# Kernel tuning notes

Measured on AMD Instinct MI355X. Metric: run time of the kernel, lower is better.

The kernel has to match this reference:

```python
import jax, jax.numpy as jnp
import numpy as np

DIM = 512
NUM_HEADS = 8
HEAD_DIM = DIM // NUM_HEADS
SCALE = HEAD_DIM ** -0.5
B, N, K_HOPS = 16, 1024, 5


def setup_inputs() -> dict:
    key = jax.random.key(0)
    ks = jax.random.split(key, 7)
    x = jax.random.normal(ks[0], (B, N, DIM), jnp.float32)
    Hstack = jax.random.uniform(ks[1], (K_HOPS, N, N), jnp.float32)
    hop_logits_attn = jax.random.normal(ks[2], (NUM_HEADS, K_HOPS), jnp.float32)
    rel_alpha = jax.random.normal(ks[3], (NUM_HEADS,), jnp.float32)
    Wqkv = jax.random.normal(ks[4], (3 * DIM, DIM), jnp.float32) * 0.02
    Wproj = jax.random.normal(ks[5], (DIM, DIM), jnp.float32) * 0.02
    bproj = jax.random.normal(ks[6], (DIM,), jnp.float32) * 0.02
    return {"x": x, "Hstack": Hstack, "hop_logits_attn": hop_logits_attn,
            "rel_alpha": rel_alpha, "Wqkv": Wqkv, "Wproj": Wproj, "bproj": bproj}


def reference(x, Hstack, hop_logits_attn, rel_alpha, Wqkv, Wproj, bproj):
    bs, n_tok, c_dim = x.shape
    # qkv projection: [B,N,3C] -> [3,B,H,N,hd]
    qkv = (x @ Wqkv.T).reshape(bs, n_tok, 3, NUM_HEADS, c_dim // NUM_HEADS)
    qkv = qkv.transpose(2, 0, 3, 1, 4)
    q, k, v = qkv[0], qkv[1], qkv[2]
    logits = jnp.einsum('bhnd,bhmd->bhnm', q, k) * SCALE  # [B,H,N,N]
    # hop-distance bias: per-head softmax mixture over K hop matrices
    w = jax.nn.softmax(hop_logits_attn, axis=-1)          # [H,K]
    B_head = jnp.einsum('hk,kij->hij', w, Hstack)          # [H,N,N]
    attn_bias = rel_alpha[:, None, None] * B_head          # [H,N,N]
    attn = jax.nn.softmax(logits + attn_bias[None], axis=-1)
    out = jnp.einsum('bhnm,bhmd->bhnd', attn, v)           # [B,H,N,hd]
    out = out.transpose(0, 2, 1, 3).reshape(bs, n_tok, c_dim)
    return out @ Wproj.T + bproj
```

## Files before the change

### kernel.cpp

```cpp
#include <hip/hip_runtime.h>
#include <hip/hip_bf16.h>
#include <hip/hip_fp16.h>
#include <stdint.h>

#define DIM   512
#define NH    8
#define HD    64
#define NB    16
#define NTOK  1024
#define KHOPS 5

typedef __attribute__((ext_vector_type(8))) short bf16x8;
typedef __attribute__((ext_vector_type(4))) float f32x4;

#define LOG2E 1.4426950408889634f

__device__ __forceinline__ unsigned short f32_to_bf16(float f) {
    unsigned int u = __builtin_bit_cast(unsigned int, f);
    unsigned int r = (u + 0x7FFFu + ((u >> 16) & 1u)) >> 16;
    return (unsigned short)r;
}

__device__ __forceinline__ float fast_exp2(float x) {
    return __builtin_amdgcn_exp2f(x);
}

#define AS1C(p) ((const __attribute__((address_space(1))) void*)(p))
#define AS3(p)  ((__attribute__((address_space(3))) void*)(p))

__global__ __launch_bounds__(256) void cvt_f32_bf16(const float* __restrict__ in,
                                                    unsigned short* __restrict__ out, int n4) {
    int i = blockIdx.x * 256 + threadIdx.x;
    if (i < n4) {
        float4 v = reinterpret_cast<const float4*>(in)[i];
        ushort4 o;
        o.x = f32_to_bf16(v.x); o.y = f32_to_bf16(v.y);
        o.z = f32_to_bf16(v.z); o.w = f32_to_bf16(v.w);
        reinterpret_cast<ushort4*>(out)[i] = o;
    }
}

__global__ __launch_bounds__(256) void transpose_f32(const float* __restrict__ in,
                                                     float* __restrict__ outp) {
    __shared__ float Ts[64][65];
    const int tid = threadIdx.x;
    const int jt = blockIdx.x, it = blockIdx.y, k = blockIdx.z;
    const float* src = in + (size_t)k * 1048576 + (size_t)(it * 64) * 1024 + jt * 64;
    float* dst = outp + (size_t)k * 1048576 + (size_t)(jt * 64) * 1024 + it * 64;
    const int r = tid >> 2, c4 = tid & 3;
#pragma unroll
    for (int t = 0; t < 4; ++t) {
        int c = (c4 + t * 4) * 4;
        float4 v = *reinterpret_cast<const float4*>(src + (size_t)r * 1024 + c);
        Ts[r][c] = v.x; Ts[r][c + 1] = v.y; Ts[r][c + 2] = v.z; Ts[r][c + 3] = v.w;
    }
    __syncthreads();
#pragma unroll
    for (int t = 0; t < 4; ++t) {
        int c = (c4 + t * 4) * 4;
        float4 v;
        v.x = Ts[c][r]; v.y = Ts[c + 1][r]; v.z = Ts[c + 2][r]; v.w = Ts[c + 3][r];
        *reinterpret_cast<float4*>(dst + (size_t)r * 1024 + c) = v;
    }
}

__global__ __launch_bounds__(256) void bias_combine(const float* __restrict__ Ht,
                                                    const float* __restrict__ hop_logits,
                                                    const float* __restrict__ rel_alpha,
                                                    uint32_t* __restrict__ biast) {
    __shared__ float coef[NH][KHOPS];
    int tid = threadIdx.x;
    if (tid < NH) {
        float m = -1e30f;
        for (int k = 0; k < KHOPS; ++k) m = fmaxf(m, hop_logits[tid * KHOPS + k]);
        float e[KHOPS]; float s = 0.f;
        for (int k = 0; k < KHOPS; ++k) {
            e[k] = fast_exp2((hop_logits[tid * KHOPS + k] - m) * LOG2E);
            s += e[k];
        }
        float ra = rel_alpha[tid] * LOG2E / s;
        for (int k = 0; k < KHOPS; ++k) coef[tid][k] = ra * e[k];
    }
    __syncthreads();
    int o2 = blockIdx.x * 256 + tid;
    int iw2  = o2 & 15;
    int j    = (o2 >> 4) & 1023;
    int it32 = (o2 >> 14) & 31;
    int h    = o2 >> 19;
    const float2* H2 = reinterpret_cast<const float2*>(Ht);
    size_t src = (size_t)j * 512 + it32 * 16 + iw2;
    float2 h0 = H2[src];
    float2 h1 = H2[524288 + src];
    float2 h2 = H2[2 * 524288 + src];
    float2 h3 = H2[3 * 524288 + src];
    float2 h4 = H2[4 * 524288 + src];
    float vx = coef[h][0] * h0.x + coef[h][1] * h1.x + coef[h][2] * h2.x +
               coef[h][3] * h3.x + coef[h][4] * h4.x;
    float vy = coef[h][0] * h0.y + coef[h][1] * h1.y + coef[h][2] * h2.y +
               coef[h][3] * h3.y + coef[h][4] * h4.y;
    __half2 hv = __floats2half2_rn(vx, vy);
    biast[o2] = __builtin_bit_cast(uint32_t, hv);
}

template <bool BF16_OUT>
__global__ __launch_bounds__(256) void gemm_bt(const unsigned short* __restrict__ A,
                                               const unsigned short* __restrict__ Bw,
                                               void* __restrict__ Cout,
                                               const float* __restrict__ cbias,
                                               int M, int Nn, int K) {
    __shared__ unsigned short As[128 * 32];
    __shared__ unsigned short Bs[128 * 32];
    const int tid  = threadIdx.x;
    const int lane = tid & 63;
    const int w    = tid >> 6;
    const int wr   = (w >> 1) * 64, wc = (w & 1) * 64;
    const int l15  = lane & 15, quad = lane >> 4;
    const int m0   = blockIdx.x * 128, n0 = blockIdx.y * 128;

    f32x4 acc[4][4];
#pragma unroll
    for (int i = 0; i < 4; ++i)
#pragma unroll
        for (int j = 0; j < 4; ++j) { acc[i][j][0] = 0.f; acc[i][j][1] = 0.f; acc[i][j][2] = 0.f; acc[i][j][3] = 0.f; }

    for (int k0 = 0; k0 < K; k0 += 32) {
        __syncthreads();
#pragma unroll
        for (int t = 0; t < 2; ++t) {
            int c = t * 256 + w * 64 + lane;
            int r = c >> 2, kh = c & 3;
            const unsigned short* ga = A  + (size_t)(m0 + r) * K + k0 + kh * 8;
            const unsigned short* gb = Bw + (size_t)(n0 + r) * K + k0 + kh * 8;
            __builtin_amdgcn_global_load_lds(AS1C(ga), AS3(&As[(t * 256 + w * 64) * 8]), 16, 0, 0);
            __builtin_amdgcn_global_load_lds(AS1C(gb), AS3(&Bs[(t * 256 + w * 64) * 8]), 16, 0, 0);
        }
        __syncthreads();
        bf16x8 af[4], bfr[4];
#pragma unroll
        for (int rt = 0; rt < 4; ++rt)
            af[rt] = *reinterpret_cast<const bf16x8*>(&As[(wr + rt * 16 + l15) * 32 + quad * 8]);
#pragma unroll
        for (int ct = 0; ct < 4; ++ct)
            bfr[ct] = *reinterpret_cast<const bf16x8*>(&Bs[(wc + ct * 16 + l15) * 32 + quad * 8]);
#pragma unroll
        for (int rt = 0; rt < 4; ++rt)
#pragma unroll
            for (int ct = 0; ct < 4; ++ct)
                acc[rt][ct] = __builtin_amdgcn_mfma_f32_16x16x32_bf16(af[rt], bfr[ct], acc[rt][ct], 0, 0, 0);
    }

    if (BF16_OUT) {
        unsigned short* C = (unsigned short*)Cout;
#pragma unroll
        for (int rt = 0; rt < 4; ++rt)
#pragma unroll
            for (int ct = 0; ct < 4; ++ct)
#pragma unroll
                for (int reg = 0; reg < 4; ++reg) {
                    int row = m0 + wr + rt * 16 + quad * 4 + reg;
                    int col = n0 + wc + ct * 16 + l15;
                    C[(size_t)row * Nn + col] = f32_to_bf16(acc[rt][ct][reg]);
                }
    } else {
        float* C = (float*)Cout;
#pragma unroll
        for (int ct = 0; ct < 4; ++ct) {
            int col = n0 + wc + ct * 16 + l15;
            float bv = cbias[col];
#pragma unroll
            for (int rt = 0; rt < 4; ++rt)
#pragma unroll
                for (int reg = 0; reg < 4; ++reg) {
                    int row = m0 + wr + rt * 16 + quad * 4 + reg;
                    C[(size_t)row * Nn + col] = acc[rt][ct][reg] + bv;
                }
        }
    }
}

__global__ __launch_bounds__(256) void transpose_v(const unsigned short* __restrict__ qkv,
                                                   unsigned short* __restrict__ vt) {
    __shared__ unsigned short Ts[64 * 66];
    const int tid = threadIdx.x;
    const int jt = blockIdx.x, h = blockIdx.y, b = blockIdx.z;
    const int j0 = jt * 64;
#pragma unroll
    for (int t = 0; t < 2; ++t) {
        int c = t * 256 + tid;
        int j = c >> 3, dh = c & 7;
        const uint32_t* g = reinterpret_cast<const uint32_t*>(
            qkv + (size_t)(b * 1024 + j0 + j) * 1536 + 1024 + h * 64 + dh * 8);
        uint32_t d0 = g[0], d1 = g[1], d2 = g[2], d3 = g[3];
        uint32_t* ls = reinterpret_cast<uint32_t*>(&Ts[j * 66 + dh * 8]);
        ls[0] = d0; ls[1] = d1; ls[2] = d2; ls[3] = d3;
    }
    __syncthreads();
#pragma unroll
    for (int t = 0; t < 2; ++t) {
        int c = t * 256 + tid;
        int d = c >> 3, jh = c & 7;
        unsigned short tmp[8];
#pragma unroll
        for (int e = 0; e < 8; ++e) tmp[e] = Ts[(jh * 8 + e) * 66 + d];
        uint32_t o0 = (uint32_t)tmp[0] | ((uint32_t)tmp[1] << 16);
        uint32_t o1 = (uint32_t)tmp[2] | ((uint32_t)tmp[3] << 16);
        uint32_t o2 = (uint32_t)tmp[4] | ((uint32_t)tmp[5] << 16);
        uint32_t o3 = (uint32_t)tmp[6] | ((uint32_t)tmp[7] << 16);
        uint32_t* gout = reinterpret_cast<uint32_t*>(
            vt + ((size_t)((b * 8 + h) * 64 + d)) * 1024 + j0 + jh * 8);
        gout[0] = o0; gout[1] = o1; gout[2] = o2; gout[3] = o3;
    }
}

__global__ __launch_bounds__(256, 3) void flash_attn(const unsigned short* __restrict__ qkv,
                                                     const unsigned short* __restrict__ vt,
                                                     const unsigned short* __restrict__ biast,
                                                     unsigned short* __restrict__ aout) {
    __shared__ unsigned short Kb[64 * 64];
    __shared__ unsigned short Vb[64 * 64];
    __shared__ unsigned short Ps[4 * 32 * 72];
    const int tid  = threadIdx.x;
    const int lane = tid & 63, w = tid >> 6;
    const int l15  = lane & 15, quad = lane >> 4;
    const int qt = blockIdx.x, h = blockIdx.y, b = blockIdx.z;
    const int i0 = qt * 128 + w * 32;
    const float kscale = 0.125f * LOG2E;
    const int l7 = l15 & 7;

    bf16x8 qf[2][2];
#pragma unroll
    for (int rt = 0; rt < 2; ++rt)
#pragma unroll
        for (int ks = 0; ks < 2; ++ks)
            qf[rt][ks] = *reinterpret_cast<const bf16x8*>(
                qkv + (size_t)(b * 1024 + i0 + rt * 16 + l15) * 1536 + h * 64 + ks * 32 + quad * 8);

    f32x4 o[2][4];
    f32x4 lacc[2];
#pragma unroll
    for (int rt = 0; rt < 2; ++rt) {
#pragma unroll
        for (int nt = 0; nt < 4; ++nt) { o[rt][nt][0] = 0.f; o[rt][nt][1] = 0.f; o[rt][nt][2] = 0.f; o[rt][nt][3] = 0.f; }
        lacc[rt][0] = 0.f; lacc[rt][1] = 0.f; lacc[rt][2] = 0.f; lacc[rt][3] = 0.f;
    }

    bf16x8 ones;
#pragma unroll
    for (int e = 0; e < 8; ++e) ones[e] = (short)0x3F80;

    const int srow = lane >> 3;
    const int gch  = (lane & 7) ^ (srow & 7);
    const unsigned short* kgbase = qkv + (size_t)b * 1024 * 1536 + 512 + h * 64 + gch * 8;
    const unsigned short* vgbase = vt + (size_t)((b * 8 + h) * 64) * 1024 + gch * 8;
    const unsigned short* bb = biast + ((size_t)(h * 32 + qt * 4 + w) * 1024) * 32 + quad * 4;
    unsigned short* ps = &Ps[w * 32 * 72];

    for (int j0 = 0; j0 < 1024; j0 += 64) {
        __syncthreads();
#pragma unroll
        for (int t = 0; t < 2; ++t) {
            int rl = w * 16 + t * 8 + srow;
            __builtin_amdgcn_global_load_lds(AS1C(kgbase + (size_t)(j0 + rl) * 1536),
                                             AS3(&Kb[(w * 16 + t * 8) * 64]), 16, 0, 0);
            __builtin_amdgcn_global_load_lds(AS1C(vgbase + (size_t)rl * 1024 + j0),
                                             AS3(&Vb[(w * 16 + t * 8) * 64]), 16, 0, 0);
        }
        uint2 bl[2][4];
#pragma unroll
        for (int rt = 0; rt < 2; ++rt)
#pragma unroll
            for (int jt = 0; jt < 4; ++jt)
                bl[rt][jt] = *reinterpret_cast<const uint2*>(
                    bb + (size_t)(j0 + jt * 16 + l15) * 32 + rt * 16);
        __syncthreads();

        f32x4 s[2][4];
#pragma unroll
        for (int rt = 0; rt < 2; ++rt)
#pragma unroll
            for (int jt = 0; jt < 4; ++jt) { s[rt][jt][0] = 0.f; s[rt][jt][1] = 0.f; s[rt][jt][2] = 0.f; s[rt][jt][3] = 0.f; }
#pragma unroll
        for (int ks = 0; ks < 2; ++ks) {
            bf16x8 kf[4];
#pragma unroll
            for (int jt = 0; jt < 4; ++jt)
                kf[jt] = *reinterpret_cast<const bf16x8*>(
                    &Kb[(jt * 16 + l15) * 64 + (((ks * 4 + quad) ^ l7) * 8)]);
#pragma unroll
            for (int rt = 0; rt < 2; ++rt)
#pragma unroll
                for (int jt = 0; jt < 4; ++jt)
                    s[rt][jt] = __builtin_amdgcn_mfma_f32_16x16x32_bf16(qf[rt][ks], kf[jt], s[rt][jt], 0, 0, 0);
        }

#pragma unroll
        for (int rt = 0; rt < 2; ++rt)
#pragma unroll
            for (int jt = 0; jt < 4; ++jt) {
                float2 f0 = __half22float2(__builtin_bit_cast(__half2, bl[rt][jt].x));
                float2 f1 = __half22float2(__builtin_bit_cast(__half2, bl[rt][jt].y));
                float bvr[4] = {f0.x, f0.y, f1.x, f1.y};
#pragma unroll
                for (int reg = 0; reg < 4; ++reg) {
                    float p = fast_exp2(__builtin_fmaf(s[rt][jt][reg], kscale, bvr[reg]));
                    ps[(rt * 16 + quad * 4 + reg) * 72 + jt * 16 + l15] = f32_to_bf16(p);
                }
            }

#pragma unroll
        for (int ks = 0; ks < 2; ++ks) {
            bf16x8 pf[2], vf[4];
#pragma unroll
            for (int rt = 0; rt < 2; ++rt)
                pf[rt] = *reinterpret_cast<const bf16x8*>(ps + (rt * 16 + l15) * 72 + ks * 32 + quad * 8);
#pragma unroll
            for (int nt = 0; nt < 4; ++nt)
                vf[nt] = *reinterpret_cast<const bf16x8*>(
                    &Vb[(nt * 16 + l15) * 64 + (((ks * 4 + quad) ^ l7) * 8)]);
#pragma unroll
            for (int rt = 0; rt < 2; ++rt) {
#pragma unroll
                for (int nt = 0; nt < 4; ++nt)
                    o[rt][nt] = __builtin_amdgcn_mfma_f32_16x16x32_bf16(pf[rt], vf[nt], o[rt][nt], 0, 0, 0);
                lacc[rt] = __builtin_amdgcn_mfma_f32_16x16x32_bf16(pf[rt], ones, lacc[rt], 0, 0, 0);
            }
        }
    }

#pragma unroll
    for (int rt = 0; rt < 2; ++rt) {
        float inv[4];
#pragma unroll
        for (int reg = 0; reg < 4; ++reg) inv[reg] = 1.f / lacc[rt][reg];
#pragma unroll
        for (int nt = 0; nt < 4; ++nt)
#pragma unroll
            for (int reg = 0; reg < 4; ++reg) {
                int row = b * 1024 + i0 + rt * 16 + quad * 4 + reg;
                int col = h * 64 + nt * 16 + l15;
                aout[(size_t)row * 512 + col] = f32_to_bf16(o[rt][nt][reg] * inv[reg]);
            }
    }
}

extern "C" void kernel_launch(void* const* d_in, const int* in_sizes, int n_in,
                              void* d_out, int out_size, void* d_ws, size_t ws_size,
                              hipStream_t stream) {
    const float* x          = (const float*)d_in[0];
    const float* Hstack     = (const float*)d_in[1];
    const float* hop_logits = (const float*)d_in[2];
    const float* rel_alpha  = (const float*)d_in[3];
    const float* Wqkv       = (const float*)d_in[4];
    const float* Wproj      = (const float*)d_in[5];
    const float* bproj      = (const float*)d_in[6];
    float* out = (float*)d_out;

    char* ws = (char*)d_ws;
    unsigned short* xb    = (unsigned short*)(ws);
    unsigned short* wqb   = (unsigned short*)(ws + 16777216);
    unsigned short* wpb   = (unsigned short*)(ws + 18350080);
    unsigned short* qkvb  = (unsigned short*)(ws + 18874368);
    unsigned short* vtb   = (unsigned short*)(ws + 69206016);
    unsigned short* biast = (unsigned short*)(ws + 85983232);
    float*          Ht    = (float*)(ws + 102760448);
    unsigned short* aoutb = (unsigned short*)(ws + 102760448);

    cvt_f32_bf16<<<8192, 256, 0, stream>>>(x, xb, 2097152);
    cvt_f32_bf16<<<768, 256, 0, stream>>>(Wqkv, wqb, 196608);
    cvt_f32_bf16<<<256, 256, 0, stream>>>(Wproj, wpb, 65536);

    transpose_f32<<<dim3(16, 16, 5), 256, 0, stream>>>(Hstack, Ht);
    bias_combine<<<16384, 256, 0, stream>>>(Ht, hop_logits, rel_alpha, (uint32_t*)biast);

    gemm_bt<true><<<dim3(128, 12), 256, 0, stream>>>(xb, wqb, qkvb, nullptr, 16384, 1536, 512);

    transpose_v<<<dim3(16, 8, 16), 256, 0, stream>>>(qkvb, vtb);

    flash_attn<<<dim3(8, 8, 16), 256, 0, stream>>>(qkvb, vtb, biast, aoutb);

    gemm_bt<false><<<dim3(128, 4), 256, 0, stream>>>(aoutb, wpb, out, bproj, 16384, 512, 512);
}
```

Before: 267.7 us.

## Fuse hop-bias transpose/combine and double-buffer K/V in larger flash-attention tiles

Merges the Hstack transpose and the per-head bias combine into a single kernel. It reads Hstack directly in its original layout and transposes the half-precision result through LDS, which avoids writing and re-reading a full fp32 transposed copy. The flash attention kernel now processes 64 query rows per wave (256 per block), halving the grid and doubling K/V reuse. It also double-buffers the K/V LDS tiles and the bias registers so the next tile's loads overlap the current tile's compute. The cost is higher register and LDS use, so occupancy drops from 3 to 2 blocks per CU, and with half as many blocks the GPU may be less full.

```diff
diff --git a/kernel.cpp b/kernel.cpp
--- a/kernel.cpp
+++ b/kernel.cpp
@@ -40,66 +40,59 @@
     }
 }
 
-__global__ __launch_bounds__(256) void transpose_f32(const float* __restrict__ in,
-                                                     float* __restrict__ outp) {
-    __shared__ float Ts[64][65];
+__global__ __launch_bounds__(256) void bias_fused(const float* __restrict__ H,
+                                                  const float* __restrict__ hop_logits,
+                                                  const float* __restrict__ rel_alpha,
+                                                  uint32_t* __restrict__ biast) {
+    __shared__ unsigned short Ls[64 * 76];
     const int tid = threadIdx.x;
-    const int jt = blockIdx.x, it = blockIdx.y, k = blockIdx.z;
-    const float* src = in + (size_t)k * 1048576 + (size_t)(it * 64) * 1024 + jt * 64;
-    float* dst = outp + (size_t)k * 1048576 + (size_t)(jt * 64) * 1024 + it * 64;
-    const int r = tid >> 2, c4 = tid & 3;
-#pragma unroll
-    for (int t = 0; t < 4; ++t) {
-        int c = (c4 + t * 4) * 4;
-        float4 v = *reinterpret_cast<const float4*>(src + (size_t)r * 1024 + c);
-        Ts[r][c] = v.x; Ts[r][c + 1] = v.y; Ts[r][c + 2] = v.z; Ts[r][c + 3] = v.w;
+    const int jt = blockIdx.x, it = blockIdx.y, h = blockIdx.z;
+    const int j0 = jt * 64, i0 = it * 64;
+    float cf[KHOPS];
+    {
+        float m = -1e30f;
+#pragma unroll
+        for (int k = 0; k < KHOPS; ++k) m = fmaxf(m, hop_logits[h * KHOPS + k]);
+        float s = 0.f;
+#pragma unroll
+        for (int k = 0; k < KHOPS; ++k) { cf[k] = fast_exp2((hop_logits[h * KHOPS + k] - m) * LOG2E); s += cf[k]; }
+        float ra = rel_alpha[h] * LOG2E / s;
+#pragma unroll
+        for (int k = 0; k < KHOPS; ++k) cf[k] *= ra;
+    }
+    const int r = tid >> 2, c0 = (tid & 3) * 16;
+    float acc[16];
+#pragma unroll
+    for (int e = 0; e < 16; ++e) acc[e] = 0.f;
+    for (int k = 0; k < KHOPS; ++k) {
+        const float4* src = reinterpret_cast<const float4*>(
+            H + (size_t)k * 1048576 + (size_t)(i0 + r) * 1024 + j0 + c0);
+#pragma unroll
+        for (int q = 0; q < 4; ++q) {
+            float4 v = src[q];
+            acc[q * 4 + 0] += cf[k] * v.x; acc[q * 4 + 1] += cf[k] * v.y;
+            acc[q * 4 + 2] += cf[k] * v.z; acc[q * 4 + 3] += cf[k] * v.w;
+        }
+    }
+#pragma unroll
+    for (int q = 0; q < 4; ++q) {
+        __half2 p0 = __floats2half2_rn(acc[q * 4 + 0], acc[q * 4 + 1]);
+        __half2 p1 = __floats2half2_rn(acc[q * 4 + 2], acc[q * 4 + 3]);
+        uint32_t* d = reinterpret_cast<uint32_t*>(&Ls[r * 76 + c0 + q * 4]);
+        d[0] = __builtin_bit_cast(uint32_t, p0);
+        d[1] = __builtin_bit_cast(uint32_t, p1);
     }
     __syncthreads();
-#pragma unroll
-    for (int t = 0; t < 4; ++t) {
-        int c = (c4 + t * 4) * 4;
-        float4 v;
-        v.x = Ts[c][r]; v.y = Ts[c + 1][r]; v.z = Ts[c + 2][r]; v.w = Ts[c + 3][r];
-        *reinterpret_cast<float4*>(dst + (size_t)r * 1024 + c) = v;
-    }
-}
-
-__global__ __launch_bounds__(256) void bias_combine(const float* __restrict__ Ht,
-                                                    const float* __restrict__ hop_logits,
-                                                    const float* __restrict__ rel_alpha,
-                                                    uint32_t* __restrict__ biast) {
-    __shared__ float coef[NH][KHOPS];
-    int tid = threadIdx.x;
-    if (tid < NH) {
-        float m = -1e30f;
-        for (int k = 0; k < KHOPS; ++k) m = fmaxf(m, hop_logits[tid * KHOPS + k]);
-        float e[KHOPS]; float s = 0.f;
-        for (int k = 0; k < KHOPS; ++k) {
-            e[k] = fast_exp2((hop_logits[tid * KHOPS + k] - m) * LOG2E);
-            s += e[k];
-        }
-        float ra = rel_alpha[tid] * LOG2E / s;
-        for (int k = 0; k < KHOPS; ++k) coef[tid][k] = ra * e[k];
-    }
-    __syncthreads();
-    int o2 = blockIdx.x * 256 + tid;
-    int iw2  = o2 & 15;
-    int j    = (o2 >> 4) & 1023;
-    int it32 = (o2 >> 14) & 31;
-    int h    = o2 >> 19;
-    const float2* H2 = reinterpret_cast<const float2*>(Ht);
-    size_t src = (size_t)j * 512 + it32 * 16 + iw2;
-    float2 h0 = H2[src];
-    float2 h1 = H2[524288 + src];
-    float2 h2 = H2[2 * 524288 + src];
-    float2 h3 = H2[3 * 524288 + src];
-    float2 h4 = H2[4 * 524288 + src];
-    float vx = coef[h][0] * h0.x + coef[h][1] * h1.x + coef[h][2] * h2.x +
-               coef[h][3] * h3.x + coef[h][4] * h4.x;
-    float vy = coef[h][0] * h0.y + coef[h][1] * h1.y + coef[h][2] * h2.y +
-               coef[h][3] * h3.y + coef[h][4] * h4.y;
-    __half2 hv = __floats2half2_rn(vx, vy);
-    biast[o2] = __builtin_bit_cast(uint32_t, hv);
+    const int iw2 = tid & 15, jl = tid >> 4;
+#pragma unroll
+    for (int g = 0; g < 2; ++g)
+#pragma unroll
+        for (int t = 0; t < 4; ++t) {
+            int j = t * 16 + jl;
+            int i = g * 32 + iw2 * 2;
+            uint32_t lo = (uint32_t)Ls[i * 76 + j] | ((uint32_t)Ls[(i + 1) * 76 + j] << 16);
+            biast[(size_t)((h * 32 + (i0 >> 5) + g) * 1024 + (j0 + j)) * 16 + iw2] = lo;
+        }
 }
 
 template <bool BF16_OUT>
@@ -212,33 +205,32 @@
     }
 }
 
-__global__ __launch_bounds__(256, 3) void flash_attn(const unsigned short* __restrict__ qkv,
+__global__ __launch_bounds__(256, 2) void flash_attn(const unsigned short* __restrict__ qkv,
                                                      const unsigned short* __restrict__ vt,
                                                      const unsigned short* __restrict__ biast,
                                                      unsigned short* __restrict__ aout) {
-    __shared__ unsigned short Kb[64 * 64];
-    __shared__ unsigned short Vb[64 * 64];
-    __shared__ unsigned short Ps[4 * 32 * 72];
+    __shared__ unsigned short Kb[2][64 * 64];
+    __shared__ unsigned short Vb[2][64 * 64];
+    __shared__ unsigned short Ps[4][64 * 72];
     const int tid  = threadIdx.x;
     const int lane = tid & 63, w = tid >> 6;
-    const int l15  = lane & 15, quad = lane >> 4;
+    const int l15  = lane & 15, quad = lane >> 4, l7 = l15 & 7;
     const int qt = blockIdx.x, h = blockIdx.y, b = blockIdx.z;
-    const int i0 = qt * 128 + w * 32;
+    const int i0 = qt * 256 + w * 64;
     const float kscale = 0.125f * LOG2E;
-    const int l7 = l15 & 7;
-
-    bf16x8 qf[2][2];
-#pragma unroll
-    for (int rt = 0; rt < 2; ++rt)
+
+    bf16x8 qf[4][2];
+#pragma unroll
+    for (int rt = 0; rt < 4; ++rt)
 #pragma unroll
         for (int ks = 0; ks < 2; ++ks)
             qf[rt][ks] = *reinterpret_cast<const bf16x8*>(
                 qkv + (size_t)(b * 1024 + i0 + rt * 16 + l15) * 1536 + h * 64 + ks * 32 + quad * 8);
 
-    f32x4 o[2][4];
-    f32x4 lacc[2];
-#pragma unroll
-    for (int rt = 0; rt < 2; ++rt) {
+    f32x4 o[4][4];
+    f32x4 lacc[4];
+#pragma unroll
+    for (int rt = 0; rt < 4; ++rt) {
 #pragma unroll
         for (int nt = 0; nt < 4; ++nt) { o[rt][nt][0] = 0.f; o[rt][nt][1] = 0.f; o[rt][nt][2] = 0.f; o[rt][nt][3] = 0.f; }
         lacc[rt][0] = 0.f; lacc[rt][1] = 0.f; lacc[rt][2] = 0.f; lacc[rt][3] = 0.f;
@@ -249,86 +241,109 @@
     for (int e = 0; e < 8; ++e) ones[e] = (short)0x3F80;
 
     const int srow = lane >> 3;
-    const int gch  = (lane & 7) ^ (srow & 7);
+    const int gch  = (lane & 7) ^ srow;
     const unsigned short* kgbase = qkv + (size_t)b * 1024 * 1536 + 512 + h * 64 + gch * 8;
     const unsigned short* vgbase = vt + (size_t)((b * 8 + h) * 64) * 1024 + gch * 8;
-    const unsigned short* bb = biast + ((size_t)(h * 32 + qt * 4 + w) * 1024) * 32 + quad * 4;
-    unsigned short* ps = &Ps[w * 32 * 72];
-
-    for (int j0 = 0; j0 < 1024; j0 += 64) {
+    const unsigned short* bb = biast + (size_t)(h * 32 + qt * 8 + w * 2) * 32768 + quad * 4;
+    unsigned short* ps = &Ps[w][0];
+
+    uint2 bl[2][4][4];
+#pragma unroll
+    for (int t = 0; t < 2; ++t) {
+        int rl = w * 16 + t * 8 + srow;
+        __builtin_amdgcn_global_load_lds(AS1C(kgbase + (size_t)rl * 1536),
+                                         AS3(&Kb[0][(w * 16 + t * 8) * 64]), 16, 0, 0);
+        __builtin_amdgcn_global_load_lds(AS1C(vgbase + (size_t)rl * 1024),
+                                         AS3(&Vb[0][(w * 16 + t * 8) * 64]), 16, 0, 0);
+    }
+#pragma unroll
+    for (int rt = 0; rt < 4; ++rt)
+#pragma unroll
+        for (int jt = 0; jt < 4; ++jt)
+            bl[0][rt][jt] = *reinterpret_cast<const uint2*>(
+                bb + (rt >> 1) * 32768 + (size_t)(jt * 16 + l15) * 32 + (rt & 1) * 16);
+
+#pragma unroll 2
+    for (int it = 0; it < 16; ++it) {
+        const int cur = it & 1, nxt = cur ^ 1;
+        const int j0 = it * 64;
         __syncthreads();
-#pragma unroll
-        for (int t = 0; t < 2; ++t) {
-            int rl = w * 16 + t * 8 + srow;
-            __builtin_amdgcn_global_load_lds(AS1C(kgbase + (size_t)(j0 + rl) * 1536),
-                                             AS3(&Kb[(w * 16 + t * 8) * 64]), 16, 0, 0);
-            __builtin_amdgcn_global_load_lds(AS1C(vgbase + (size_t)rl * 1024 + j0),
-                                             AS3(&Vb[(w * 16 + t * 8) * 64]), 16, 0, 0);
-        }
-        uint2 bl[2][4];
-#pragma unroll
-        for (int rt = 0; rt < 2; ++rt)
-#pragma unroll
-            for (int jt = 0; jt < 4; ++jt)
-                bl[rt][jt] = *reinterpret_cast<const uint2*>(
-                    bb + (size_t)(j0 + jt * 16 + l15) * 32 + rt * 16);
-        __syncthreads();
-
-        f32x4 s[2][4];
-#pragma unroll
-        for (int rt = 0; rt < 2; ++rt)
-#pragma unroll
-            for (int jt = 0; jt < 4; ++jt) { s[rt][jt][0] = 0.f; s[rt][jt][1] = 0.f; s[rt][jt][2] = 0.f; s[rt][jt][3] = 0.f; }
+
+        if (it < 15) {
+            const int j0n = j0 + 64;
+#pragma unroll
+            for (int t = 0; t < 2; ++t) {
+                int rl = w * 16 + t * 8 + srow;
+                __builtin_amdgcn_global_load_lds(AS1C(kgbase + (size_t)(j0n + rl) * 1536),
+                                                 AS3(&Kb[nxt][(w * 16 + t * 8) * 64]), 16, 0, 0);
+                __builtin_amdgcn_global_load_lds(AS1C(vgbase + (size_t)rl * 1024 + j0n),
+                                                 AS3(&Vb[nxt][(w * 16 + t * 8) * 64]), 16, 0, 0);
+            }
+#pragma unroll
+            for (int rt = 0; rt < 4; ++rt)
+#pragma unroll
+                for (int jt = 0; jt < 4; ++jt)
+                    bl[nxt][rt][jt] = *reinterpret_cast<const uint2*>(
+                        bb + (rt >> 1) * 32768 + (size_t)(j0n + jt * 16 + l15) * 32 + (rt & 1) * 16);
+        }
+
+#pragma unroll
+        for (int rth = 0; rth < 2; ++rth) {
+            f32x4 s[2][4];
+#pragma unroll
+            for (int r2 = 0; r2 < 2; ++r2)
+#pragma unroll
+                for (int jt = 0; jt < 4; ++jt) { s[r2][jt][0] = 0.f; s[r2][jt][1] = 0.f; s[r2][jt][2] = 0.f; s[r2][jt][3] = 0.f; }
+#pragma unroll
+            for (int ks = 0; ks < 2; ++ks) {
+                bf16x8 kf[4];
+#pragma unroll
+                for (int jt = 0; jt < 4; ++jt)
+                    kf[jt] = *reinterpret_cast<const bf16x8*>(
+                        &Kb[cur][(jt * 16 + l15) * 64 + (((ks * 4 + quad) ^ l7) * 8)]);
+#pragma unroll
+                for (int r2 = 0; r2 < 2; ++r2)
+#pragma unroll
+                    for (int jt = 0; jt < 4; ++jt)
+                        s[r2][jt] = __builtin_amdgcn_mfma_f32_16x16x32_bf16(qf[rth * 2 + r2][ks], kf[jt], s[r2][jt], 0, 0, 0);
+            }
+#pragma unroll
+            for (int r2 = 0; r2 < 2; ++r2) {
+                const int rt = rth * 2 + r2;
+#pragma unroll
+                for (int jt = 0; jt < 4; ++jt) {
+                    float2 f0 = __half22float2(__builtin_bit_cast(__half2, bl[cur][rt][jt].x));
+                    float2 f1 = __half22float2(__builtin_bit_cast(__half2, bl[cur][rt][jt].y));
+                    float bvr[4] = {f0.x, f0.y, f1.x, f1.y};
+#pragma unroll
+                    for (int reg = 0; reg < 4; ++reg) {
+                        float p = fast_exp2(__builtin_fmaf(s[r2][jt][reg], kscale, bvr[reg]));
+                        ps[(rt * 16 + quad * 4 + reg) * 72 + jt * 16 + l15] = f32_to_bf16(p);
+                    }
+                }
+            }
+        }
+
 #pragma unroll
         for (int ks = 0; ks < 2; ++ks) {
-            bf16x8 kf[4];
-#pragma unroll
-            for (int jt = 0; jt < 4; ++jt)
-                kf[jt] = *reinterpret_cast<const bf16x8*>(
-                    &Kb[(jt * 16 + l15) * 64 + (((ks * 4 + quad) ^ l7) * 8)]);
-#pragma unroll
-            for (int rt = 0; rt < 2; ++rt)
-#pragma unroll
-                for (int jt = 0; jt < 4; ++jt)
-                    s[rt][jt] = __builtin_amdgcn_mfma_f32_16x16x32_bf16(qf[rt][ks], kf[jt], s[rt][jt], 0, 0, 0);
-        }
-
-#pragma unroll
-        for (int rt = 0; rt < 2; ++rt)
-#pragma unroll
-            for (int jt = 0; jt < 4; ++jt) {
-                float2 f0 = __half22float2(__builtin_bit_cast(__half2, bl[rt][jt].x));
-                float2 f1 = __half22float2(__builtin_bit_cast(__half2, bl[rt][jt].y));
-                float bvr[4] = {f0.x, f0.y, f1.x, f1.y};
-#pragma unroll
-                for (int reg = 0; reg < 4; ++reg) {
-                    float p = fast_exp2(__builtin_fmaf(s[rt][jt][reg], kscale, bvr[reg]));
-                    ps[(rt * 16 + quad * 4 + reg) * 72 + jt * 16 + l15] = f32_to_bf16(p);
-                }
-            }
-
-#pragma unroll
-        for (int ks = 0; ks < 2; ++ks) {
-            bf16x8 pf[2], vf[4];
-#pragma unroll
-            for (int rt = 0; rt < 2; ++rt)
-                pf[rt] = *reinterpret_cast<const bf16x8*>(ps + (rt * 16 + l15) * 72 + ks * 32 + quad * 8);
+            bf16x8 vf[4];
 #pragma unroll
             for (int nt = 0; nt < 4; ++nt)
                 vf[nt] = *reinterpret_cast<const bf16x8*>(
-                    &Vb[(nt * 16 + l15) * 64 + (((ks * 4 + quad) ^ l7) * 8)]);
-#pragma unroll
-            for (int rt = 0; rt < 2; ++rt) {
+                    &Vb[cur][(nt * 16 + l15) * 64 + (((ks * 4 + quad) ^ l7) * 8)]);
+#pragma unroll
+            for (int rt = 0; rt < 4; ++rt) {
+                bf16x8 pf = *reinterpret_cast<const bf16x8*>(ps + (rt * 16 + l15) * 72 + ks * 32 + quad * 8);
 #pragma unroll
                 for (int nt = 0; nt < 4; ++nt)
-                    o[rt][nt] = __builtin_amdgcn_mfma_f32_16x16x32_bf16(pf[rt], vf[nt], o[rt][nt], 0, 0, 0);
-                lacc[rt] = __builtin_amdgcn_mfma_f32_16x16x32_bf16(pf[rt], ones, lacc[rt], 0, 0, 0);
-            }
-        }
-    }
-
-#pragma unroll
-    for (int rt = 0; rt < 2; ++rt) {
+                    o[rt][nt] = __builtin_amdgcn_mfma_f32_16x16x32_bf16(pf, vf[nt], o[rt][nt], 0, 0, 0);
+                lacc[rt] = __builtin_amdgcn_mfma_f32_16x16x32_bf16(pf, ones, lacc[rt], 0, 0, 0);
+            }
+        }
+    }
+
+#pragma unroll
+    for (int rt = 0; rt < 4; ++rt) {
         float inv[4];
 #pragma unroll
         for (int reg = 0; reg < 4; ++reg) inv[reg] = 1.f / lacc[rt][reg];
@@ -362,21 +377,19 @@
     unsigned short* qkvb  = (unsigned short*)(ws + 18874368);
     unsigned short* vtb   = (unsigned short*)(ws + 69206016);
     unsigned short* biast = (unsigned short*)(ws + 85983232);
-    float*          Ht    = (float*)(ws + 102760448);
     unsigned short* aoutb = (unsigned short*)(ws + 102760448);
 
     cvt_f32_bf16<<<8192, 256, 0, stream>>>(x, xb, 2097152);
     cvt_f32_bf16<<<768, 256, 0, stream>>>(Wqkv, wqb, 196608);
     cvt_f32_bf16<<<256, 256, 0, stream>>>(Wproj, wpb, 65536);
 
-    transpose_f32<<<dim3(16, 16, 5), 256, 0, stream>>>(Hstack, Ht);
-    bias_combine<<<16384, 256, 0, stream>>>(Ht, hop_logits, rel_alpha, (uint32_t*)biast);
+    bias_fused<<<dim3(16, 16, 8), 256, 0, stream>>>(Hstack, hop_logits, rel_alpha, (uint32_t*)biast);
 
     gemm_bt<true><<<dim3(128, 12), 256, 0, stream>>>(xb, wqb, qkvb, nullptr, 16384, 1536, 512);
 
     transpose_v<<<dim3(16, 8, 16), 256, 0, stream>>>(qkvb, vtb);
 
-    flash_attn<<<dim3(8, 8, 16), 256, 0, stream>>>(qkvb, vtb, biast, aoutb);
+    flash_attn<<<dim3(4, 8, 16), 256, 0, stream>>>(qkvb, vtb, biast, aoutb);
 
     gemm_bt<false><<<dim3(128, 4), 256, 0, stream>>>(aoutb, wpb, out, bproj, 16384, 512, 512);
 }
```

Result: slower. 273.1 us (+2.0%).

## Fuse conversion kernels, bias transpose-combine, and V transpose into GEMM epilogue

Applied to the files above, without the earlier changes.

Merges the three fp32-to-bf16 conversion launches into one kernel and replaces the Hstack transpose plus bias combine with a single tiled kernel. That kernel reads Hstack directly, mixes the hops per head in registers and transposes through LDS. The QKV GEMM now writes the V columns directly in transposed layout, removing the separate transpose_v pass and its extra read and write of V. The flash attention grid is reordered so head is the fastest-varying block index, which may improve bias and cache locality. Fewer launches and intermediate buffers remain, at the cost of strided 8-byte stores in the V epilogue, and bias_fused now rereads Hstack once per head.

```diff
diff --git a/kernel.cpp b/kernel.cpp
--- a/kernel.cpp
+++ b/kernel.cpp
@@ -28,86 +28,83 @@
 #define AS1C(p) ((const __attribute__((address_space(1))) void*)(p))
 #define AS3(p)  ((__attribute__((address_space(3))) void*)(p))
 
-__global__ __launch_bounds__(256) void cvt_f32_bf16(const float* __restrict__ in,
-                                                    unsigned short* __restrict__ out, int n4) {
-    int i = blockIdx.x * 256 + threadIdx.x;
-    if (i < n4) {
-        float4 v = reinterpret_cast<const float4*>(in)[i];
-        ushort4 o;
-        o.x = f32_to_bf16(v.x); o.y = f32_to_bf16(v.y);
-        o.z = f32_to_bf16(v.z); o.w = f32_to_bf16(v.w);
-        reinterpret_cast<ushort4*>(out)[i] = o;
-    }
-}
-
-__global__ __launch_bounds__(256) void transpose_f32(const float* __restrict__ in,
-                                                     float* __restrict__ outp) {
-    __shared__ float Ts[64][65];
+__global__ __launch_bounds__(256) void cvt_all(const float* __restrict__ x,
+                                               const float* __restrict__ wq,
+                                               const float* __restrict__ wp,
+                                               unsigned short* __restrict__ xb,
+                                               unsigned short* __restrict__ wqb,
+                                               unsigned short* __restrict__ wpb) {
+    int bid = blockIdx.x;
+    const float* in; unsigned short* out; int i;
+    if (bid < 8192)      { in = x;  out = xb;  i = bid * 256 + threadIdx.x; }
+    else if (bid < 8960) { in = wq; out = wqb; i = (bid - 8192) * 256 + threadIdx.x; }
+    else                 { in = wp; out = wpb; i = (bid - 8960) * 256 + threadIdx.x; }
+    float4 v = reinterpret_cast<const float4*>(in)[i];
+    ushort4 o;
+    o.x = f32_to_bf16(v.x); o.y = f32_to_bf16(v.y);
+    o.z = f32_to_bf16(v.z); o.w = f32_to_bf16(v.w);
+    reinterpret_cast<ushort4*>(out)[i] = o;
+}
+
+__global__ __launch_bounds__(256) void bias_fused(const float* __restrict__ H,
+                                                  const float* __restrict__ hop_logits,
+                                                  const float* __restrict__ rel_alpha,
+                                                  uint32_t* __restrict__ biast) {
+    __shared__ unsigned short Ls[64 * 76];
     const int tid = threadIdx.x;
-    const int jt = blockIdx.x, it = blockIdx.y, k = blockIdx.z;
-    const float* src = in + (size_t)k * 1048576 + (size_t)(it * 64) * 1024 + jt * 64;
-    float* dst = outp + (size_t)k * 1048576 + (size_t)(jt * 64) * 1024 + it * 64;
-    const int r = tid >> 2, c4 = tid & 3;
-#pragma unroll
-    for (int t = 0; t < 4; ++t) {
-        int c = (c4 + t * 4) * 4;
-        float4 v = *reinterpret_cast<const float4*>(src + (size_t)r * 1024 + c);
-        Ts[r][c] = v.x; Ts[r][c + 1] = v.y; Ts[r][c + 2] = v.z; Ts[r][c + 3] = v.w;
+    const int jt = blockIdx.x, it = blockIdx.y, h = blockIdx.z;
+    const int j0 = jt * 64, i0 = it * 64;
+    float cf[KHOPS];
+    {
+        float m = -1e30f;
+#pragma unroll
+        for (int k = 0; k < KHOPS; ++k) m = fmaxf(m, hop_logits[h * KHOPS + k]);
+        float s = 0.f;
+#pragma unroll
+        for (int k = 0; k < KHOPS; ++k) { cf[k] = fast_exp2((hop_logits[h * KHOPS + k] - m) * LOG2E); s += cf[k]; }
+        float ra = rel_alpha[h] * LOG2E / s;
+#pragma unroll
+        for (int k = 0; k < KHOPS; ++k) cf[k] *= ra;
+    }
+    const int r = tid >> 2, c0 = (tid & 3) * 16;
+    float acc[16];
+#pragma unroll
+    for (int e = 0; e < 16; ++e) acc[e] = 0.f;
+    for (int k = 0; k < KHOPS; ++k) {
+        const float4* src = reinterpret_cast<const float4*>(
+            H + (size_t)k * 1048576 + (size_t)(i0 + r) * 1024 + j0 + c0);
+#pragma unroll
+        for (int q = 0; q < 4; ++q) {
+            float4 v = src[q];
+            acc[q * 4 + 0] += cf[k] * v.x; acc[q * 4 + 1] += cf[k] * v.y;
+            acc[q * 4 + 2] += cf[k] * v.z; acc[q * 4 + 3] += cf[k] * v.w;
+        }
+    }
+#pragma unroll
+    for (int q = 0; q < 4; ++q) {
+        __half2 p0 = __floats2half2_rn(acc[q * 4 + 0], acc[q * 4 + 1]);
+        __half2 p1 = __floats2half2_rn(acc[q * 4 + 2], acc[q * 4 + 3]);
+        uint32_t* d = reinterpret_cast<uint32_t*>(&Ls[r * 76 + c0 + q * 4]);
+        d[0] = __builtin_bit_cast(uint32_t, p0);
+        d[1] = __builtin_bit_cast(uint32_t, p1);
     }
     __syncthreads();
-#pragma unroll
-    for (int t = 0; t < 4; ++t) {
-        int c = (c4 + t * 4) * 4;
-        float4 v;
-        v.x = Ts[c][r]; v.y = Ts[c + 1][r]; v.z = Ts[c + 2][r]; v.w = Ts[c + 3][r];
-        *reinterpret_cast<float4*>(dst + (size_t)r * 1024 + c) = v;
-    }
-}
-
-__global__ __launch_bounds__(256) void bias_combine(const float* __restrict__ Ht,
-                                                    const float* __restrict__ hop_logits,
-                                                    const float* __restrict__ rel_alpha,
-                                                    uint32_t* __restrict__ biast) {
-    __shared__ float coef[NH][KHOPS];
-    int tid = threadIdx.x;
-    if (tid < NH) {
-        float m = -1e30f;
-        for (int k = 0; k < KHOPS; ++k) m = fmaxf(m, hop_logits[tid * KHOPS + k]);
-        float e[KHOPS]; float s = 0.f;
-        for (int k = 0; k < KHOPS; ++k) {
-            e[k] = fast_exp2((hop_logits[tid * KHOPS + k] - m) * LOG2E);
-            s += e[k];
-        }
-        float ra = rel_alpha[tid] * LOG2E / s;
-        for (int k = 0; k < KHOPS; ++k) coef[tid][k] = ra * e[k];
-    }
-    __syncthreads();
-    int o2 = blockIdx.x * 256 + tid;
-    int iw2  = o2 & 15;
-    int j    = (o2 >> 4) & 1023;
-    int it32 = (o2 >> 14) & 31;
-    int h    = o2 >> 19;
-    const float2* H2 = reinterpret_cast<const float2*>(Ht);
-    size_t src = (size_t)j * 512 + it32 * 16 + iw2;
-    float2 h0 = H2[src];
-    float2 h1 = H2[524288 + src];
-    float2 h2 = H2[2 * 524288 + src];
-    float2 h3 = H2[3 * 524288 + src];
-    float2 h4 = H2[4 * 524288 + src];
-    float vx = coef[h][0] * h0.x + coef[h][1] * h1.x + coef[h][2] * h2.x +
-               coef[h][3] * h3.x + coef[h][4] * h4.x;
-    float vy = coef[h][0] * h0.y + coef[h][1] * h1.y + coef[h][2] * h2.y +
-               coef[h][3] * h3.y + coef[h][4] * h4.y;
-    __half2 hv = __floats2half2_rn(vx, vy);
-    biast[o2] = __builtin_bit_cast(uint32_t, hv);
-}
-
-template <bool BF16_OUT>
-__global__ __launch_bounds__(256) void gemm_bt(const unsigned short* __restrict__ A,
-                                               const unsigned short* __restrict__ Bw,
-                                               void* __restrict__ Cout,
-                                               const float* __restrict__ cbias,
-                                               int M, int Nn, int K) {
+    const int iw2 = tid & 15, jl = tid >> 4;
+#pragma unroll
+    for (int g = 0; g < 2; ++g)
+#pragma unroll
+        for (int t = 0; t < 4; ++t) {
+            int j = t * 16 + jl;
+            int i = g * 32 + iw2 * 2;
+            uint32_t lo = (uint32_t)Ls[i * 76 + j] | ((uint32_t)Ls[(i + 1) * 76 + j] << 16);
+            biast[(size_t)((h * 32 + (i0 >> 5) + g) * 1024 + (j0 + j)) * 16 + iw2] = lo;
+        }
+}
+
+__global__ __launch_bounds__(256) void gemm_qkv(const unsigned short* __restrict__ A,
+                                                const unsigned short* __restrict__ Bw,
+                                                unsigned short* __restrict__ qkv,
+                                                unsigned short* __restrict__ vt) {
     __shared__ unsigned short As[128 * 32];
     __shared__ unsigned short Bs[128 * 32];
     const int tid  = threadIdx.x;
@@ -116,6 +113,7 @@
     const int wr   = (w >> 1) * 64, wc = (w & 1) * 64;
     const int l15  = lane & 15, quad = lane >> 4;
     const int m0   = blockIdx.x * 128, n0 = blockIdx.y * 128;
+    const int K = 512, Nn = 1536;
 
     f32x4 acc[4][4];
 #pragma unroll
@@ -149,8 +147,7 @@
                 acc[rt][ct] = __builtin_amdgcn_mfma_f32_16x16x32_bf16(af[rt], bfr[ct], acc[rt][ct], 0, 0, 0);
     }
 
-    if (BF16_OUT) {
-        unsigned short* C = (unsigned short*)Cout;
+    if (n0 < 1024) {
 #pragma unroll
         for (int rt = 0; rt < 4; ++rt)
 #pragma unroll
@@ -159,56 +156,85 @@
                 for (int reg = 0; reg < 4; ++reg) {
                     int row = m0 + wr + rt * 16 + quad * 4 + reg;
                     int col = n0 + wc + ct * 16 + l15;
-                    C[(size_t)row * Nn + col] = f32_to_bf16(acc[rt][ct][reg]);
+                    qkv[(size_t)row * Nn + col] = f32_to_bf16(acc[rt][ct][reg]);
                 }
     } else {
-        float* C = (float*)Cout;
+        const int b = m0 >> 10;
 #pragma unroll
         for (int ct = 0; ct < 4; ++ct) {
-            int col = n0 + wc + ct * 16 + l15;
-            float bv = cbias[col];
-#pragma unroll
-            for (int rt = 0; rt < 4; ++rt)
-#pragma unroll
-                for (int reg = 0; reg < 4; ++reg) {
-                    int row = m0 + wr + rt * 16 + quad * 4 + reg;
-                    C[(size_t)row * Nn + col] = acc[rt][ct][reg] + bv;
-                }
-        }
-    }
-}
-
-__global__ __launch_bounds__(256) void transpose_v(const unsigned short* __restrict__ qkv,
-                                                   unsigned short* __restrict__ vt) {
-    __shared__ unsigned short Ts[64 * 66];
-    const int tid = threadIdx.x;
-    const int jt = blockIdx.x, h = blockIdx.y, b = blockIdx.z;
-    const int j0 = jt * 64;
-#pragma unroll
-    for (int t = 0; t < 2; ++t) {
-        int c = t * 256 + tid;
-        int j = c >> 3, dh = c & 7;
-        const uint32_t* g = reinterpret_cast<const uint32_t*>(
-            qkv + (size_t)(b * 1024 + j0 + j) * 1536 + 1024 + h * 64 + dh * 8);
-        uint32_t d0 = g[0], d1 = g[1], d2 = g[2], d3 = g[3];
-        uint32_t* ls = reinterpret_cast<uint32_t*>(&Ts[j * 66 + dh * 8]);
-        ls[0] = d0; ls[1] = d1; ls[2] = d2; ls[3] = d3;
-    }
-    __syncthreads();
-#pragma unroll
-    for (int t = 0; t < 2; ++t) {
-        int c = t * 256 + tid;
-        int d = c >> 3, jh = c & 7;
-        unsigned short tmp[8];
-#pragma unroll
-        for (int e = 0; e < 8; ++e) tmp[e] = Ts[(jh * 8 + e) * 66 + d];
-        uint32_t o0 = (uint32_t)tmp[0] | ((uint32_t)tmp[1] << 16);
-        uint32_t o1 = (uint32_t)tmp[2] | ((uint32_t)tmp[3] << 16);
-        uint32_t o2 = (uint32_t)tmp[4] | ((uint32_t)tmp[5] << 16);
-        uint32_t o3 = (uint32_t)tmp[6] | ((uint32_t)tmp[7] << 16);
-        uint32_t* gout = reinterpret_cast<uint32_t*>(
-            vt + ((size_t)((b * 8 + h) * 64 + d)) * 1024 + j0 + jh * 8);
-        gout[0] = o0; gout[1] = o1; gout[2] = o2; gout[3] = o3;
+            int c = n0 - 1024 + wc + ct * 16 + l15;
+            unsigned short* vrow = vt + ((size_t)(b * 8) * 64 + c) * 1024;
+#pragma unroll
+            for (int rt = 0; rt < 4; ++rt) {
+                int trow = (m0 & 1023) + wr + rt * 16 + quad * 4;
+                ushort4 pk;
+                pk.x = f32_to_bf16(acc[rt][ct][0]);
+                pk.y = f32_to_bf16(acc[rt][ct][1]);
+                pk.z = f32_to_bf16(acc[rt][ct][2]);
+                pk.w = f32_to_bf16(acc[rt][ct][3]);
+                *reinterpret_cast<ushort4*>(vrow + trow) = pk;
+            }
+        }
+    }
+}
+
+__global__ __launch_bounds__(256) void gemm_proj(const unsigned short* __restrict__ A,
+                                                 const unsigned short* __restrict__ Bw,
+                                                 float* __restrict__ C,
+                                                 const float* __restrict__ cbias,
+                                                 int M, int Nn, int K) {
+    __shared__ unsigned short As[128 * 32];
+    __shared__ unsigned short Bs[128 * 32];
+    const int tid  = threadIdx.x;
+    const int lane = tid & 63;
+    const int w    = tid >> 6;
+    const int wr   = (w >> 1) * 64, wc = (w & 1) * 64;
+    const int l15  = lane & 15, quad = lane >> 4;
+    const int m0   = blockIdx.x * 128, n0 = blockIdx.y * 128;
+
+    f32x4 acc[4][4];
+#pragma unroll
+    for (int i = 0; i < 4; ++i)
+#pragma unroll
+        for (int j = 0; j < 4; ++j) { acc[i][j][0] = 0.f; acc[i][j][1] = 0.f; acc[i][j][2] = 0.f; acc[i][j][3] = 0.f; }
+
+    for (int k0 = 0; k0 < K; k0 += 32) {
+        __syncthreads();
+#pragma unroll
+        for (int t = 0; t < 2; ++t) {
+            int c = t * 256 + w * 64 + lane;
+            int r = c >> 2, kh = c & 3;
+            const unsigned short* ga = A  + (size_t)(m0 + r) * K + k0 + kh * 8;
+            const unsigned short* gb = Bw + (size_t)(n0 + r) * K + k0 + kh * 8;
+            __builtin_amdgcn_global_load_lds(AS1C(ga), AS3(&As[(t * 256 + w * 64) * 8]), 16, 0, 0);
+            __builtin_amdgcn_global_load_lds(AS1C(gb), AS3(&Bs[(t * 256 + w * 64) * 8]), 16, 0, 0);
+        }
+        __syncthreads();
+        bf16x8 af[4], bfr[4];
+#pragma unroll
+        for (int rt = 0; rt < 4; ++rt)
+            af[rt] = *reinterpret_cast<const bf16x8*>(&As[(wr + rt * 16 + l15) * 32 + quad * 8]);
+#pragma unroll
+        for (int ct = 0; ct < 4; ++ct)
+            bfr[ct] = *reinterpret_cast<const bf16x8*>(&Bs[(wc + ct * 16 + l15) * 32 + quad * 8]);
+#pragma unroll
+        for (int rt = 0; rt < 4; ++rt)
+#pragma unroll
+            for (int ct = 0; ct < 4; ++ct)
+                acc[rt][ct] = __builtin_amdgcn_mfma_f32_16x16x32_bf16(af[rt], bfr[ct], acc[rt][ct], 0, 0, 0);
+    }
+
+#pragma unroll
+    for (int ct = 0; ct < 4; ++ct) {
+        int col = n0 + wc + ct * 16 + l15;
+        float bv = cbias[col];
+#pragma unroll
+        for (int rt = 0; rt < 4; ++rt)
+#pragma unroll
+            for (int reg = 0; reg < 4; ++reg) {
+                int row = m0 + wr + rt * 16 + quad * 4 + reg;
+                C[(size_t)row * Nn + col] = acc[rt][ct][reg] + bv;
+            }
     }
 }
 
@@ -222,7 +248,7 @@
     const int tid  = threadIdx.x;
     const int lane = tid & 63, w = tid >> 6;
     const int l15  = lane & 15, quad = lane >> 4;
-    const int qt = blockIdx.x, h = blockIdx.y, b = blockIdx.z;
+    const int h = blockIdx.x, qt = blockIdx.y, b = blockIdx.z;
     const int i0 = qt * 128 + w * 32;
     const float kscale = 0.125f * LOG2E;
     const int l7 = l15 & 7;
@@ -362,21 +388,15 @@
     unsigned short* qkvb  = (unsigned short*)(ws + 18874368);
     unsigned short* vtb   = (unsigned short*)(ws + 69206016);
     unsigned short* biast = (unsigned short*)(ws + 85983232);
-    float*          Ht    = (float*)(ws + 102760448);
     unsigned short* aoutb = (unsigned short*)(ws + 102760448);
 
-    cvt_f32_bf16<<<8192, 256, 0, stream>>>(x, xb, 2097152);
-    cvt_f32_bf16<<<768, 256, 0, stream>>>(Wqkv, wqb, 196608);
-    cvt_f32_bf16<<<256, 256, 0, stream>>>(Wproj, wpb, 65536);
-
-    transpose_f32<<<dim3(16, 16, 5), 256, 0, stream>>>(Hstack, Ht);
-    bias_combine<<<16384, 256, 0, stream>>>(Ht, hop_logits, rel_alpha, (uint32_t*)biast);
-
-    gemm_bt<true><<<dim3(128, 12), 256, 0, stream>>>(xb, wqb, qkvb, nullptr, 16384, 1536, 512);
-
-    transpose_v<<<dim3(16, 8, 16), 256, 0, stream>>>(qkvb, vtb);
+    cvt_all<<<9216, 256, 0, stream>>>(x, Wqkv, Wproj, xb, wqb, wpb);
+
+    bias_fused<<<dim3(16, 16, 8), 256, 0, stream>>>(Hstack, hop_logits, rel_alpha, (uint32_t*)biast);
+
+    gemm_qkv<<<dim3(128, 12), 256, 0, stream>>>(xb, wqb, qkvb, vtb);
 
     flash_attn<<<dim3(8, 8, 16), 256, 0, stream>>>(qkvb, vtb, biast, aoutb);
 
-    gemm_bt<false><<<dim3(128, 4), 256, 0, stream>>>(aoutb, wpb, out, bproj, 16384, 512, 512);
-}
+    gemm_proj<<<dim3(128, 4), 256, 0, stream>>>(aoutb, wpb, out, bproj, 16384, 512, 512);
+}
```

Result: faster. 255.2 us (-4.7%).
